# Performance work log

Hardware: AMD Instinct MI355X
Metric: run time of the kernel (lower is better)

The kernel has to match this reference:

```python
import jax, jax.numpy as jnp
import numpy as np

N_NODES = 100000
N_EDGES = 1600000
IN_CH = 128
TYPE_EMB = 32
OUT_CH = 128
N_REL = 8
N_BASES = 8
N_NTYPES = 8
FEAT = IN_CH + TYPE_EMB  # 160, RGCNConv input dim after concat


def setup_inputs() -> dict:
    key = jax.random.key(0)
    ks = jax.random.split(key, 9)
    x = jax.random.normal(ks[0], (N_NODES, IN_CH), dtype=jnp.float32)
    node_type_ids = jax.random.randint(ks[1], (N_NODES,), 0, N_NTYPES)
    edge_index = jax.random.randint(ks[2], (2, N_EDGES), 0, N_NODES)
    edge_type = jax.random.randint(ks[3], (N_EDGES,), 0, N_REL)
    emb_table = jax.random.normal(ks[4], (N_NTYPES, TYPE_EMB), dtype=jnp.float32)
    bases = jax.random.normal(ks[5], (N_BASES, FEAT, OUT_CH), dtype=jnp.float32) * (1.0 / np.sqrt(FEAT))
    comp = jax.random.normal(ks[6], (N_REL, N_BASES), dtype=jnp.float32) * (1.0 / np.sqrt(N_BASES))
    root_w = jax.random.normal(ks[7], (FEAT, OUT_CH), dtype=jnp.float32) * (1.0 / np.sqrt(FEAT))
    bias = jnp.zeros((OUT_CH,), dtype=jnp.float32)
    return {"x": x, "node_type_ids": node_type_ids, "edge_index": edge_index,
            "edge_type": edge_type, "emb_table": emb_table, "bases": bases,
            "comp": comp, "root_w": root_w, "bias": bias}


def reference(x, node_type_ids, edge_index, edge_type, emb_table, bases, comp, root_w, bias):
    N = x.shape[0]
    # node-type embedding lookup + concat
    h = jnp.concatenate([x, emb_table[node_type_ids]], axis=1)  # [N, FEAT]
    # basis decomposition: per-relation weights [R, FEAT, OUT]
    weight = jnp.einsum('rb,bio->rio', comp, bases)
    src, dst = edge_index[0], edge_index[1]
    h_src = h[src]  # [E, FEAT] -- dominant gather
    # root/self transform + bias
    out = h @ root_w + bias
    # PyG RGCNConv default aggr='mean': per-relation mean over incoming edges, summed across relations
    for r in range(weight.shape[0]):
        m = (edge_type == r).astype(h.dtype)  # [E]
        s = jax.ops.segment_sum(h_src * m[:, None], dst, num_segments=N)  # [N, FEAT]
        c = jax.ops.segment_sum(m, dst, num_segments=N)                    # [N]
        mean_r = s / jnp.maximum(c, 1.0)[:, None]
        out = out + mean_r @ weight[r]
    # dropout is identity in eval mode
    return jax.nn.relu(out)
```

## Files before the change

kernel.cpp:

```cpp
#include <hip/hip_runtime.h>

#define NN 100000
#define NE 1600000
#define INC 128
#define TE 32
#define OC 128
#define NR 8
#define NBASES 8
#define FT 160
#define KP 168
#define KW 160
#define TN 64
#define NBKT 1563
#define NB1 782
#define EPB 2048
#define CAP 1536

typedef float f32x4 __attribute__((ext_vector_type(4)));
typedef __bf16 bf16x8 __attribute__((ext_vector_type(8)));

__device__ __forceinline__ unsigned f2bf1(float f) {
    unsigned u = __float_as_uint(f);
    return (u + 0x7fffu + ((u >> 16) & 1u)) >> 16;
}
__device__ __forceinline__ float bf2f(unsigned s) { return __uint_as_float(s << 16); }

__device__ __forceinline__ int bscan_excl(int v, int* tmp) {
    int tid = threadIdx.x;
    tmp[tid] = v; __syncthreads();
#pragma unroll
    for (int d = 1; d < 256; d <<= 1) {
        int t = (tid >= d) ? tmp[tid - d] : 0;
        __syncthreads();
        tmp[tid] += t;
        __syncthreads();
    }
    return tmp[tid] - v;
}

__global__ void k_wt(const float* __restrict__ comp, const float* __restrict__ bases,
                     const float* __restrict__ rootw, unsigned short* __restrict__ Wt) {
    int idx = blockIdx.x * 256 + threadIdx.x;
    const int tot = 9 * 128 * KW;
    if (idx >= tot) return;
    int ridx = idx / (128 * KW);
    int rem  = idx % (128 * KW);
    int o = rem / KW;
    int k = rem % KW;
    float v;
    if (ridx < NR) {
        v = 0.f;
#pragma unroll
        for (int b = 0; b < NBASES; b++)
            v += comp[ridx * NBASES + b] * bases[(b * FT + k) * OC + o];
    } else {
        v = rootw[k * OC + o];
    }
    Wt[idx] = (unsigned short)f2bf1(v);
}

__global__ void k_h(const float* __restrict__ x, const int* __restrict__ nt,
                    const float* __restrict__ emb, unsigned short* __restrict__ h) {
    int idx = blockIdx.x * 256 + threadIdx.x;
    if (idx >= NN * 20) return;
    int n = idx / 20, c = idx % 20;
    f32x4 v0, v1;
    if (c < 16) {
        const float* p = x + (size_t)n * INC + c * 8;
        v0 = *(const f32x4*)p; v1 = *(const f32x4*)(p + 4);
    } else {
        int tt = nt[n];
        const float* p = emb + tt * TE + (c - 16) * 8;
        v0 = *(const f32x4*)p; v1 = *(const f32x4*)(p + 4);
    }
    uint4 o;
    o.x = f2bf1(v0.x) | (f2bf1(v0.y) << 16);
    o.y = f2bf1(v0.z) | (f2bf1(v0.w) << 16);
    o.z = f2bf1(v1.x) | (f2bf1(v1.y) << 16);
    o.w = f2bf1(v1.z) | (f2bf1(v1.w) << 16);
    *(uint4*)(h + (size_t)n * FT + c * 8) = o;
}

__global__ __launch_bounds__(256) void k_hist1(const int* __restrict__ ei, int* __restrict__ ghist) {
    __shared__ int hist[NBKT];
    int tid = threadIdx.x;
    for (int j = tid; j < NBKT; j += 256) hist[j] = 0;
    __syncthreads();
    int e0 = blockIdx.x * EPB;
#pragma unroll
    for (int k = 0; k < EPB / 256; k++) {
        int e = e0 + k * 256 + tid;
        if (e < NE) atomicAdd(&hist[ei[NE + e] >> 6], 1);
    }
    __syncthreads();
    int* g = ghist + (size_t)blockIdx.x * NBKT;
    for (int j = tid; j < NBKT; j += 256) g[j] = hist[j];
}

__global__ void k_total(const int* __restrict__ ghist, int* __restrict__ total) {
    __shared__ int tmp[256];
    int j = blockIdx.x, tid = threadIdx.x, s = 0;
    for (int b = tid; b < NB1; b += 256) s += ghist[(size_t)b * NBKT + j];
    tmp[tid] = s; __syncthreads();
#pragma unroll
    for (int k = 128; k > 0; k >>= 1) { if (tid < k) tmp[tid] += tmp[tid + k]; __syncthreads(); }
    if (tid == 0) total[j] = tmp[0];
}

__global__ void k_scanTot(const int* __restrict__ total, int* __restrict__ bstart) {
    __shared__ int tmp[256];
    int tid = threadIdx.x, s = 0, i0 = tid * 7;
#pragma unroll
    for (int i = 0; i < 7; i++) { int j = i0 + i; if (j < NBKT) s += total[j]; }
    int run = bscan_excl(s, tmp);
#pragma unroll
    for (int i = 0; i < 7; i++) { int j = i0 + i; if (j < NBKT) { bstart[j] = run; run += total[j]; } }
    if (tid == 0) bstart[NBKT] = NE;
}

__global__ void k_offsets(int* __restrict__ ghist, const int* __restrict__ bstart) {
    __shared__ int tmp[256];
    int j = blockIdx.x, tid = threadIdx.x, s = 0, b0 = tid * 4;
    int loc[4];
#pragma unroll
    for (int i = 0; i < 4; i++) {
        int b = b0 + i;
        loc[i] = (b < NB1) ? ghist[(size_t)b * NBKT + j] : 0;
        s += loc[i];
    }
    int run = bscan_excl(s, tmp) + bstart[j];
#pragma unroll
    for (int i = 0; i < 4; i++) {
        int b = b0 + i;
        if (b < NB1) { ghist[(size_t)b * NBKT + j] = run; run += loc[i]; }
    }
}

__global__ __launch_bounds__(256) void k_scatter1(const int* __restrict__ ei, const int* __restrict__ et,
                                                  const int* __restrict__ ghist, unsigned* __restrict__ slots) {
    __shared__ int cur[NBKT];
    int tid = threadIdx.x, b = blockIdx.x;
    for (int j = tid; j < NBKT; j += 256) cur[j] = ghist[(size_t)b * NBKT + j];
    __syncthreads();
    int e0 = b * EPB;
#pragma unroll
    for (int k = 0; k < EPB / 256; k++) {
        int e = e0 + k * 256 + tid;
        if (e < NE) {
            int s = ei[e], d = ei[NE + e], r = et[e];
            int pos = atomicAdd(&cur[d >> 6], 1);
            slots[pos] = (unsigned)s | ((unsigned)r << 17) | ((unsigned)(d & 63) << 20);
        }
    }
}

__global__ __launch_bounds__(256) void k_sort2(unsigned* __restrict__ slots, const int* __restrict__ bstart,
                                               unsigned* __restrict__ pk) {
    __shared__ unsigned buf[CAP], buf2[CAP];
    __shared__ int hist[512], base[512], cur[512], tmp[256];
    int j = blockIdx.x, tid = threadIdx.x;
    int s0 = bstart[j];
    int n = bstart[j + 1] - s0; if (n > CAP) n = CAP;
    for (int i = tid; i < n; i += 256) buf[i] = slots[s0 + i];
    for (int k = tid; k < 512; k += 256) hist[k] = 0;
    __syncthreads();
    for (int i = tid; i < n; i += 256) {
        unsigned v = buf[i];
        int key = (int)(((v >> 17) & 7u) * 64u + ((v >> 20) & 63u));
        atomicAdd(&hist[key], 1);
    }
    __syncthreads();
    int v0 = hist[2 * tid], v1 = hist[2 * tid + 1];
    int ex = bscan_excl(v0 + v1, tmp);
    base[2 * tid] = ex;      base[2 * tid + 1] = ex + v0;
    cur[2 * tid]  = ex;      cur[2 * tid + 1]  = ex + v0;
    __syncthreads();
    for (int k = tid; k < 512; k += 256)
        pk[(size_t)j * 512 + k] = (unsigned)base[k] | ((unsigned)hist[k] << 16);
    for (int i = tid; i < n; i += 256) {
        unsigned v = buf[i];
        int key = (int)(((v >> 17) & 7u) * 64u + ((v >> 20) & 63u));
        int p = atomicAdd(&cur[key], 1);
        buf2[p] = v & 0x03F1FFFFu;
    }
    __syncthreads();
    for (int i = tid; i < n; i += 256) slots[s0 + i] = buf2[i];
}

__global__ __launch_bounds__(256, 4) void k_mega(
    const unsigned short* __restrict__ h, const float* __restrict__ bias,
    const unsigned short* __restrict__ Wt, const unsigned* __restrict__ pk,
    const int* __restrict__ bstart, const unsigned* __restrict__ slots,
    float* __restrict__ out) {
    __shared__ unsigned short feat[TN * KP];
    __shared__ unsigned sl[CAP];
    __shared__ unsigned pkl[512];

    const int tid = threadIdx.x;
    const int lane = tid & 63;
    const int wave = tid >> 6;
    const int j = blockIdx.x;
    const int n0 = j * TN;

    int s0 = bstart[j];
    int m = bstart[j + 1] - s0; if (m > CAP) m = CAP;
    for (int i = tid; i < m; i += 256) sl[i] = slots[s0 + i];
    for (int k = tid; k < 512; k += 256) pkl[k] = pk[(size_t)j * 512 + k];

    for (int i = tid; i < TN * 20; i += 256) {
        int nl = i / 20, c = i % 20, n = n0 + nl;
        uint4 v = (uint4){0u, 0u, 0u, 0u};
        if (n < NN) v = *reinterpret_cast<const uint4*>(h + (size_t)n * FT + c * 8);
        *reinterpret_cast<uint4*>(&feat[nl * KP + c * 8]) = v;
    }

    f32x4 acc[8];
#pragma unroll
    for (int t = 0; t < 8; t++) acc[t] = (f32x4){0.f, 0.f, 0.f, 0.f};

    auto mfma_pass = [&](int ridx) {
        const unsigned short* fA = feat + (lane & 15) * KP + ((lane >> 4) * 8);
        const unsigned short* gB = Wt + (size_t)ridx * 128 * KW
                                   + (wave * 32 + (lane & 15)) * KW + ((lane >> 4) * 8);
#pragma unroll
        for (int kc = 0; kc < 5; kc++) {
            bf16x8 a0 = *reinterpret_cast<const bf16x8*>(fA + 0 * 16 * KP + kc * 32);
            bf16x8 a1 = *reinterpret_cast<const bf16x8*>(fA + 1 * 16 * KP + kc * 32);
            bf16x8 a2 = *reinterpret_cast<const bf16x8*>(fA + 2 * 16 * KP + kc * 32);
            bf16x8 a3 = *reinterpret_cast<const bf16x8*>(fA + 3 * 16 * KP + kc * 32);
#pragma unroll
            for (int ct = 0; ct < 2; ct++) {
                bf16x8 b = *reinterpret_cast<const bf16x8*>(gB + ct * 16 * KW + kc * 32);
                acc[0 * 2 + ct] = __builtin_amdgcn_mfma_f32_16x16x32_bf16(a0, b, acc[0 * 2 + ct], 0, 0, 0);
                acc[1 * 2 + ct] = __builtin_amdgcn_mfma_f32_16x16x32_bf16(a1, b, acc[1 * 2 + ct], 0, 0, 0);
                acc[2 * 2 + ct] = __builtin_amdgcn_mfma_f32_16x16x32_bf16(a2, b, acc[2 * 2 + ct], 0, 0, 0);
                acc[3 * 2 + ct] = __builtin_amdgcn_mfma_f32_16x16x32_bf16(a3, b, acc[3 * 2 + ct], 0, 0, 0);
            }
        }
    };

    __syncthreads();
    mfma_pass(8);

    const int g = tid >> 4, l = tid & 15;
    const unsigned* hw = reinterpret_cast<const unsigned*>(h);
    for (int r = 0; r < NR; r++) {
        __syncthreads();
        int b0 = r * 64 + 4 * g;
        for (int q = 0; q < 4; q++) {
            unsigned p = pkl[b0 + q];
            int off = (int)(p & 0xffffu);
            int cnt = (int)(p >> 16);
            float sa[10];
#pragma unroll
            for (int i = 0; i < 10; i++) sa[i] = 0.f;
            if (cnt > 0) {
                unsigned cur[5];
                const unsigned* hp = hw + (size_t)(sl[off] & 0x1FFFFu) * 80 + l;
#pragma unroll
                for (int c = 0; c < 5; c++) cur[c] = hp[c * 16];
                for (int e = 0; e < cnt; e++) {
                    int en = (e + 1 < cnt) ? e + 1 : e;
                    const unsigned* hp2 = hw + (size_t)(sl[off + en] & 0x1FFFFu) * 80 + l;
                    unsigned nx[5];
#pragma unroll
                    for (int c = 0; c < 5; c++) nx[c] = hp2[c * 16];
#pragma unroll
                    for (int c = 0; c < 5; c++) {
                        sa[2 * c]     += bf2f(cur[c] & 0xffffu);
                        sa[2 * c + 1] += bf2f(cur[c] >> 16);
                        cur[c] = nx[c];
                    }
                }
            }
            float inv = (cnt > 0) ? (1.0f / (float)cnt) : 0.f;
            unsigned* fp = reinterpret_cast<unsigned*>(&feat[(4 * g + q) * KP]) + l;
#pragma unroll
            for (int c = 0; c < 5; c++)
                fp[c * 16] = f2bf1(sa[2 * c] * inv) | (f2bf1(sa[2 * c + 1] * inv) << 16);
        }
        __syncthreads();
        mfma_pass(r);
    }

    const int rq = lane >> 4;
#pragma unroll
    for (int ct = 0; ct < 2; ct++) {
        int col = wave * 32 + ct * 16 + (lane & 15);
        float bv = bias[col];
#pragma unroll
        for (int rt = 0; rt < 4; rt++) {
#pragma unroll
            for (int i = 0; i < 4; i++) {
                int n = n0 + rt * 16 + rq * 4 + i;
                if (n < NN) {
                    float v = acc[rt * 2 + ct][i] + bv;
                    out[(size_t)n * OC + col] = v > 0.f ? v : 0.f;
                }
            }
        }
    }
}

extern "C" void kernel_launch(void* const* d_in, const int* in_sizes, int n_in,
                              void* d_out, int out_size, void* d_ws, size_t ws_size,
                              hipStream_t stream) {
    const float* x     = (const float*)d_in[0];
    const int*   ntype = (const int*)d_in[1];
    const int*   ei    = (const int*)d_in[2];
    const int*   et    = (const int*)d_in[3];
    const float* emb   = (const float*)d_in[4];
    const float* bases = (const float*)d_in[5];
    const float* comp  = (const float*)d_in[6];
    const float* rootw = (const float*)d_in[7];
    const float* bias  = (const float*)d_in[8];
    float* out = (float*)d_out;

    char* ws = (char*)d_ws;
    unsigned short* Wt     = (unsigned short*)(ws);
    unsigned short* h      = (unsigned short*)(ws + 368640);
    int*            ghist  = (int*)(ws + 32368640);
    int*            total  = (int*)(ws + 37257728);
    int*            bstart = (int*)(ws + 37264128);
    unsigned*       pk     = (unsigned*)(ws + 37270528);
    unsigned*       slots  = (unsigned*)(ws + 40471552);

    k_wt      <<<720,   256, 0, stream>>>(comp, bases, rootw, Wt);
    k_h       <<<7813,  256, 0, stream>>>(x, ntype, emb, h);
    k_hist1   <<<NB1,   256, 0, stream>>>(ei, ghist);
    k_total   <<<NBKT,  256, 0, stream>>>(ghist, total);
    k_scanTot <<<1,     256, 0, stream>>>(total, bstart);
    k_offsets <<<NBKT,  256, 0, stream>>>(ghist, bstart);
    k_scatter1<<<NB1,   256, 0, stream>>>(ei, et, ghist, slots);
    k_sort2   <<<NBKT,  256, 0, stream>>>(slots, bstart, pk);
    k_mega    <<<NBKT,  256, 0, stream>>>(h, bias, Wt, pk, bstart, slots, out);
}
```

Baseline: 373.9 us.

## Fuse prep kernels and bucket sort into mega kernel, merge per-node aggregation loops

Merges the weight and feature preparation kernels into one launch, cuts histogram chunks to 512 and makes the total and offset passes serial per thread, and folds the second-level sort into the main kernel so the sorted slot array and pk table never round-trip through global memory. Each wave's gather loop now walks all edges for its four destination nodes in one run, flushing whenever the destination changes, so the gather pipeline is not restarted per node. The launch-bounds occupancy hint rises from 4 to 5. In exchange the main kernel does more shared-memory sorting work and may use registers less freely, and the total and offset kernels run on only 7 blocks.

New measurement: 372.4 us. No clear change (-0.4%).

```diff
diff --git a/kernel.cpp b/kernel.cpp
--- a/kernel.cpp
+++ b/kernel.cpp
@@ -12,8 +12,8 @@
 #define KW 160
 #define TN 64
 #define NBKT 1563
-#define NB1 782
-#define EPB 2048
+#define NCH 512
+#define EPB 3125
 #define CAP 1536
 
 typedef float f32x4 __attribute__((ext_vector_type(4)));
@@ -23,7 +23,6 @@
     unsigned u = __float_as_uint(f);
     return (u + 0x7fffu + ((u >> 16) & 1u)) >> 16;
 }
-__device__ __forceinline__ float bf2f(unsigned s) { return __uint_as_float(s << 16); }
 
 __device__ __forceinline__ int bscan_excl(int v, int* tmp) {
     int tid = threadIdx.x;
@@ -38,59 +37,57 @@
     return tmp[tid] - v;
 }
 
-__global__ void k_wt(const float* __restrict__ comp, const float* __restrict__ bases,
-                     const float* __restrict__ rootw, unsigned short* __restrict__ Wt) {
+__global__ void k_prep(const float* __restrict__ x, const int* __restrict__ nt,
+                       const float* __restrict__ emb, const float* __restrict__ comp,
+                       const float* __restrict__ bases, const float* __restrict__ rootw,
+                       unsigned short* __restrict__ h, unsigned short* __restrict__ Wt) {
     int idx = blockIdx.x * 256 + threadIdx.x;
-    const int tot = 9 * 128 * KW;
-    if (idx >= tot) return;
-    int ridx = idx / (128 * KW);
-    int rem  = idx % (128 * KW);
-    int o = rem / KW;
-    int k = rem % KW;
-    float v;
-    if (ridx < NR) {
-        v = 0.f;
-#pragma unroll
-        for (int b = 0; b < NBASES; b++)
-            v += comp[ridx * NBASES + b] * bases[(b * FT + k) * OC + o];
-    } else {
-        v = rootw[k * OC + o];
-    }
-    Wt[idx] = (unsigned short)f2bf1(v);
-}
-
-__global__ void k_h(const float* __restrict__ x, const int* __restrict__ nt,
-                    const float* __restrict__ emb, unsigned short* __restrict__ h) {
-    int idx = blockIdx.x * 256 + threadIdx.x;
-    if (idx >= NN * 20) return;
-    int n = idx / 20, c = idx % 20;
-    f32x4 v0, v1;
-    if (c < 16) {
-        const float* p = x + (size_t)n * INC + c * 8;
-        v0 = *(const f32x4*)p; v1 = *(const f32x4*)(p + 4);
-    } else {
-        int tt = nt[n];
-        const float* p = emb + tt * TE + (c - 16) * 8;
-        v0 = *(const f32x4*)p; v1 = *(const f32x4*)(p + 4);
-    }
-    uint4 o;
-    o.x = f2bf1(v0.x) | (f2bf1(v0.y) << 16);
-    o.y = f2bf1(v0.z) | (f2bf1(v0.w) << 16);
-    o.z = f2bf1(v1.x) | (f2bf1(v1.y) << 16);
-    o.w = f2bf1(v1.z) | (f2bf1(v1.w) << 16);
-    *(uint4*)(h + (size_t)n * FT + c * 8) = o;
-}
-
-__global__ __launch_bounds__(256) void k_hist1(const int* __restrict__ ei, int* __restrict__ ghist) {
+    if (idx < 9 * 128 * KW) {
+        int ridx = idx / (128 * KW);
+        int rem  = idx % (128 * KW);
+        int o = rem / KW;
+        int k = rem % KW;
+        float v;
+        if (ridx < NR) {
+            v = 0.f;
+#pragma unroll
+            for (int b = 0; b < NBASES; b++)
+                v += comp[ridx * NBASES + b] * bases[(b * FT + k) * OC + o];
+        } else {
+            v = rootw[k * OC + o];
+        }
+        Wt[idx] = (unsigned short)f2bf1(v);
+    }
+    if (idx < NN * 20) {
+        int n = idx / 20, c = idx % 20;
+        f32x4 v0, v1;
+        if (c < 16) {
+            const float* p = x + (size_t)n * INC + c * 8;
+            v0 = *(const f32x4*)p; v1 = *(const f32x4*)(p + 4);
+        } else {
+            int tt = nt[n];
+            const float* p = emb + tt * TE + (c - 16) * 8;
+            v0 = *(const f32x4*)p; v1 = *(const f32x4*)(p + 4);
+        }
+        uint4 o;
+        o.x = f2bf1(v0.x) | (f2bf1(v0.y) << 16);
+        o.y = f2bf1(v0.z) | (f2bf1(v0.w) << 16);
+        o.z = f2bf1(v1.x) | (f2bf1(v1.y) << 16);
+        o.w = f2bf1(v1.z) | (f2bf1(v1.w) << 16);
+        *(uint4*)(h + (size_t)n * FT + c * 8) = o;
+    }
+}
+
+__global__ __launch_bounds__(256) void k_hist(const int* __restrict__ ei, int* __restrict__ ghist) {
     __shared__ int hist[NBKT];
     int tid = threadIdx.x;
     for (int j = tid; j < NBKT; j += 256) hist[j] = 0;
     __syncthreads();
     int e0 = blockIdx.x * EPB;
 #pragma unroll
-    for (int k = 0; k < EPB / 256; k++) {
-        int e = e0 + k * 256 + tid;
-        if (e < NE) atomicAdd(&hist[ei[NE + e] >> 6], 1);
+    for (int k = 0; k < 13; k++) {
+        int i = k * 256 + tid;
+        if (i < EPB) atomicAdd(&hist[ei[NE + e0 + i] >> 6], 1);
     }
     __syncthreads();
     int* g = ghist + (size_t)blockIdx.x * NBKT;
@@ -98,13 +95,12 @@
 }
 
 __global__ void k_total(const int* __restrict__ ghist, int* __restrict__ total) {
-    __shared__ int tmp[256];
-    int j = blockIdx.x, tid = threadIdx.x, s = 0;
-    for (int b = tid; b < NB1; b += 256) s += ghist[(size_t)b * NBKT + j];
-    tmp[tid] = s; __syncthreads();
-#pragma unroll
-    for (int k = 128; k > 0; k >>= 1) { if (tid < k) tmp[tid] += tmp[tid + k]; __syncthreads(); }
-    if (tid == 0) total[j] = tmp[0];
+    int j = blockIdx.x * 256 + threadIdx.x;
+    if (j >= NBKT) return;
+    int s = 0;
+#pragma unroll 8
+    for (int b = 0; b < NCH; b++) s += ghist[(size_t)b * NBKT + j];
+    total[j] = s;
 }
 
 __global__ void k_scanTot(const int* __restrict__ total, int* __restrict__ bstart) {
@@ -119,34 +115,29 @@
 }
 
 __global__ void k_offsets(int* __restrict__ ghist, const int* __restrict__ bstart) {
-    __shared__ int tmp[256];
-    int j = blockIdx.x, tid = threadIdx.x, s = 0, b0 = tid * 4;
-    int loc[4];
-#pragma unroll
-    for (int i = 0; i < 4; i++) {
-        int b = b0 + i;
-        loc[i] = (b < NB1) ? ghist[(size_t)b * NBKT + j] : 0;
-        s += loc[i];
-    }
-    int run = bscan_excl(s, tmp) + bstart[j];
-#pragma unroll
-    for (int i = 0; i < 4; i++) {
-        int b = b0 + i;
-        if (b < NB1) { ghist[(size_t)b * NBKT + j] = run; run += loc[i]; }
-    }
-}
-
-__global__ __launch_bounds__(256) void k_scatter1(const int* __restrict__ ei, const int* __restrict__ et,
-                                                  const int* __restrict__ ghist, unsigned* __restrict__ slots) {
+    int j = blockIdx.x * 256 + threadIdx.x;
+    if (j >= NBKT) return;
+    int run = bstart[j];
+#pragma unroll 4
+    for (int b = 0; b < NCH; b++) {
+        int v = ghist[(size_t)b * NBKT + j];
+        ghist[(size_t)b * NBKT + j] = run;
+        run += v;
+    }
+}
+
+__global__ __launch_bounds__(256) void k_scatter(const int* __restrict__ ei, const int* __restrict__ et,
+                                                 const int* __restrict__ ghist, unsigned* __restrict__ slots) {
     __shared__ int cur[NBKT];
     int tid = threadIdx.x, b = blockIdx.x;
     for (int j = tid; j < NBKT; j += 256) cur[j] = ghist[(size_t)b * NBKT + j];
     __syncthreads();
     int e0 = b * EPB;
 #pragma unroll
-    for (int k = 0; k < EPB / 256; k++) {
-        int e = e0 + k * 256 + tid;
-        if (e < NE) {
+    for (int k = 0; k < 13; k++) {
+        int i = k * 256 + tid;
+        if (i < EPB) {
+            int e = e0 + i;
             int s = ei[e], d = ei[NE + e], r = et[e];
             int pos = atomicAdd(&cur[d >> 6], 1);
             slots[pos] = (unsigned)s | ((unsigned)r << 17) | ((unsigned)(d & 63) << 20);
@@ -154,45 +145,11 @@
     }
 }
 
-__global__ __launch_bounds__(256) void k_sort2(unsigned* __restrict__ slots, const int* __restrict__ bstart,
-                                               unsigned* __restrict__ pk) {
-    __shared__ unsigned buf[CAP], buf2[CAP];
-    __shared__ int hist[512], base[512], cur[512], tmp[256];
-    int j = blockIdx.x, tid = threadIdx.x;
-    int s0 = bstart[j];
-    int n = bstart[j + 1] - s0; if (n > CAP) n = CAP;
-    for (int i = tid; i < n; i += 256) buf[i] = slots[s0 + i];
-    for (int k = tid; k < 512; k += 256) hist[k] = 0;
-    __syncthreads();
-    for (int i = tid; i < n; i += 256) {
-        unsigned v = buf[i];
-        int key = (int)(((v >> 17) & 7u) * 64u + ((v >> 20) & 63u));
-        atomicAdd(&hist[key], 1);
-    }
-    __syncthreads();
-    int v0 = hist[2 * tid], v1 = hist[2 * tid + 1];
-    int ex = bscan_excl(v0 + v1, tmp);
-    base[2 * tid] = ex;      base[2 * tid + 1] = ex + v0;
-    cur[2 * tid]  = ex;      cur[2 * tid + 1]  = ex + v0;
-    __syncthreads();
-    for (int k = tid; k < 512; k += 256)
-        pk[(size_t)j * 512 + k] = (unsigned)base[k] | ((unsigned)hist[k] << 16);
-    for (int i = tid; i < n; i += 256) {
-        unsigned v = buf[i];
-        int key = (int)(((v >> 17) & 7u) * 64u + ((v >> 20) & 63u));
-        int p = atomicAdd(&cur[key], 1);
-        buf2[p] = v & 0x03F1FFFFu;
-    }
-    __syncthreads();
-    for (int i = tid; i < n; i += 256) slots[s0 + i] = buf2[i];
-}
-
-__global__ __launch_bounds__(256, 4) void k_mega(
+__global__ __launch_bounds__(256, 5) void k_mega(
     const unsigned short* __restrict__ h, const float* __restrict__ bias,
-    const unsigned short* __restrict__ Wt, const unsigned* __restrict__ pk,
-    const int* __restrict__ bstart, const unsigned* __restrict__ slots,
-    float* __restrict__ out) {
-    __shared__ unsigned short feat[TN * KP];
+    const unsigned short* __restrict__ Wt, const int* __restrict__ bstart,
+    const unsigned* __restrict__ slots, float* __restrict__ out) {
+    __shared__ unsigned short featmem[TN * KP];
     __shared__ unsigned sl[CAP];
     __shared__ unsigned pkl[512];
 
@@ -202,16 +159,38 @@
     const int j = blockIdx.x;
     const int n0 = j * TN;
 
+    unsigned* sl_in = reinterpret_cast<unsigned*>(featmem);
+    int* hist = reinterpret_cast<int*>(featmem) + CAP;
+    int* tmp  = reinterpret_cast<int*>(featmem) + CAP + 512;
+
     int s0 = bstart[j];
     int m = bstart[j + 1] - s0; if (m > CAP) m = CAP;
-    for (int i = tid; i < m; i += 256) sl[i] = slots[s0 + i];
-    for (int k = tid; k < 512; k += 256) pkl[k] = pk[(size_t)j * 512 + k];
+    for (int i = tid; i < m; i += 256) sl_in[i] = slots[s0 + i];
+    for (int k = tid; k < 512; k += 256) hist[k] = 0;
+    __syncthreads();
+    for (int i = tid; i < m; i += 256) {
+        unsigned v = sl_in[i];
+        atomicAdd(&hist[((v >> 17) & 7u) * 64u + ((v >> 20) & 63u)], 1);
+    }
+    __syncthreads();
+    int v0 = hist[2 * tid], v1 = hist[2 * tid + 1];
+    int ex = bscan_excl(v0 + v1, tmp);
+    pkl[2 * tid]     = (unsigned)ex | ((unsigned)v0 << 16);
+    pkl[2 * tid + 1] = (unsigned)(ex + v0) | ((unsigned)v1 << 16);
+    hist[2 * tid] = ex; hist[2 * tid + 1] = ex + v0;
+    __syncthreads();
+    for (int i = tid; i < m; i += 256) {
+        unsigned v = sl_in[i];
+        int p = atomicAdd(&hist[((v >> 17) & 7u) * 64u + ((v >> 20) & 63u)], 1);
+        sl[p] = v & 0x03F1FFFFu;
+    }
+    __syncthreads();
 
     for (int i = tid; i < TN * 20; i += 256) {
         int nl = i / 20, c = i % 20, n = n0 + nl;
         uint4 v = (uint4){0u, 0u, 0u, 0u};
         if (n < NN) v = *reinterpret_cast<const uint4*>(h + (size_t)n * FT + c * 8);
-        *reinterpret_cast<uint4*>(&feat[nl * KP + c * 8]) = v;
+        *reinterpret_cast<uint4*>(&featmem[nl * KP + c * 8]) = v;
     }
 
     f32x4 acc[8];
@@ -219,7 +198,7 @@
     for (int t = 0; t < 8; t++) acc[t] = (f32x4){0.f, 0.f, 0.f, 0.f};
 
     auto mfma_pass = [&](int ridx) {
-        const unsigned short* fA = feat + (lane & 15) * KP + ((lane >> 4) * 8);
+        const unsigned short* fA = featmem + (lane & 15) * KP + ((lane >> 4) * 8);
         const unsigned short* gB = Wt + (size_t)ridx * 128 * KW
                                    + (wave * 32 + (lane & 15)) * KW + ((lane >> 4) * 8);
 #pragma unroll
@@ -247,37 +226,57 @@
     for (int r = 0; r < NR; r++) {
         __syncthreads();
         int b0 = r * 64 + 4 * g;
+        unsigned pa = pkl[b0], pd = pkl[b0 + 3];
+        int sbeg = (int)(pa & 0xffffu);
+        int send = (int)(pd & 0xffffu) + (int)(pd >> 16);
+        float sa[10];
+#pragma unroll
+        for (int i = 0; i < 10; i++) sa[i] = 0.f;
+        float run = 0.f;
+        unsigned cur5[5]; int curdl = 0;
+        if (sbeg < send) {
+            unsigned v = sl[sbeg];
+            const unsigned* hp = hw + (size_t)(v & 0x1FFFFu) * 80 + l;
+#pragma unroll
+            for (int c = 0; c < 5; c++) cur5[c] = hp[c * 16];
+            curdl = (int)((v >> 20) & 63u);
+        }
+        for (int e = sbeg; e < send; e++) {
+            int en = (e + 1 < send) ? e + 1 : e;
+            unsigned vn = sl[en];
+            const unsigned* hp = hw + (size_t)(vn & 0x1FFFFu) * 80 + l;
+            unsigned nx[5];
+#pragma unroll
+            for (int c = 0; c < 5; c++) nx[c] = hp[c * 16];
+            int nxdl = (int)((vn >> 20) & 63u);
+#pragma unroll
+            for (int c = 0; c < 5; c++) {
+                sa[2 * c]     += __uint_as_float(cur5[c] << 16);
+                sa[2 * c + 1] += __uint_as_float(cur5[c] & 0xFFFF0000u);
+            }
+            run += 1.f;
+            bool fl = (e + 1 >= send) || (nxdl != curdl);
+            if (fl) {
+                float inv = 1.0f / run;
+                unsigned* fp = reinterpret_cast<unsigned*>(featmem + curdl * KP) + l;
+#pragma unroll
+                for (int c = 0; c < 5; c++)
+                    fp[c * 16] = f2bf1(sa[2 * c] * inv) | (f2bf1(sa[2 * c + 1] * inv) << 16);
+#pragma unroll
+                for (int i = 0; i < 10; i++) sa[i] = 0.f;
+                run = 0.f;
+            }
+#pragma unroll
+            for (int c = 0; c < 5; c++) cur5[c] = nx[c];
+            curdl = nxdl;
+        }
+#pragma unroll
         for (int q = 0; q < 4; q++) {
-            unsigned p = pkl[b0 + q];
-            int off = (int)(p & 0xffffu);
-            int cnt = (int)(p >> 16);
-            float sa[10];
-#pragma unroll
-            for (int i = 0; i < 10; i++) sa[i] = 0.f;
-            if (cnt > 0) {
-                unsigned cur[5];
-                const unsigned* hp = hw + (size_t)(sl[off] & 0x1FFFFu) * 80 + l;
-#pragma unroll
-                for (int c = 0; c < 5; c++) cur[c] = hp[c * 16];
-                for (int e = 0; e < cnt; e++) {
-                    int en = (e + 1 < cnt) ? e + 1 : e;
-                    const unsigned* hp2 = hw + (size_t)(sl[off + en] & 0x1FFFFu) * 80 + l;
-                    unsigned nx[5];
-#pragma unroll
-                    for (int c = 0; c < 5; c++) nx[c] = hp2[c * 16];
-#pragma unroll
-                    for (int c = 0; c < 5; c++) {
-                        sa[2 * c]     += bf2f(cur[c] & 0xffffu);
-                        sa[2 * c + 1] += bf2f(cur[c] >> 16);
-                        cur[c] = nx[c];
-                    }
-                }
-            }
-            float inv = (cnt > 0) ? (1.0f / (float)cnt) : 0.f;
-            unsigned* fp = reinterpret_cast<unsigned*>(&feat[(4 * g + q) * KP]) + l;
-#pragma unroll
-            for (int c = 0; c < 5; c++)
-                fp[c * 16] = f2bf1(sa[2 * c] * inv) | (f2bf1(sa[2 * c + 1] * inv) << 16);
+            if ((pkl[b0 + q] >> 16) == 0u) {
+                unsigned* fp = reinterpret_cast<unsigned*>(featmem + (4 * g + q) * KP) + l;
+#pragma unroll
+                for (int c = 0; c < 5; c++) fp[c * 16] = 0u;
+            }
         }
         __syncthreads();
         mfma_pass(r);
@@ -320,18 +319,15 @@
     unsigned short* Wt     = (unsigned short*)(ws);
     unsigned short* h      = (unsigned short*)(ws + 368640);
     int*            ghist  = (int*)(ws + 32368640);
-    int*            total  = (int*)(ws + 37257728);
-    int*            bstart = (int*)(ws + 37264128);
-    unsigned*       pk     = (unsigned*)(ws + 37270528);
-    unsigned*       slots  = (unsigned*)(ws + 40471552);
-
-    k_wt      <<<720,   256, 0, stream>>>(comp, bases, rootw, Wt);
-    k_h       <<<7813,  256, 0, stream>>>(x, ntype, emb, h);
-    k_hist1   <<<NB1,   256, 0, stream>>>(ei, ghist);
-    k_total   <<<NBKT,  256, 0, stream>>>(ghist, total);
-    k_scanTot <<<1,     256, 0, stream>>>(total, bstart);
-    k_offsets <<<NBKT,  256, 0, stream>>>(ghist, bstart);
-    k_scatter1<<<NB1,   256, 0, stream>>>(ei, et, ghist, slots);
-    k_sort2   <<<NBKT,  256, 0, stream>>>(slots, bstart, pk);
-    k_mega    <<<NBKT,  256, 0, stream>>>(h, bias, Wt, pk, bstart, slots, out);
-}
+    int*            total  = (int*)(ws + 35569664);
+    int*            bstart = (int*)(ws + 35576064);
+    unsigned*       slots  = (unsigned*)(ws + 35582464);
+
+    k_prep   <<<7813, 256, 0, stream>>>(x, ntype, emb, comp, bases, rootw, h, Wt);
+    k_hist   <<<NCH,  256, 0, stream>>>(ei, ghist);
+    k_total  <<<7,    256, 0, stream>>>(ghist, total);
+    k_scanTot<<<1,    256, 0, stream>>>(total, bstart);
+    k_offsets<<<7,    256, 0, stream>>>(ghist, bstart);
+    k_scatter<<<NCH,  256, 0, stream>>>(ei, et, ghist, slots);
+    k_mega   <<<NBKT, 256, 0, stream>>>(h, bias, Wt, bstart, slots, out);
+}
```
